# Performance work log

Hardware: AMD Instinct MI355X
Metric: run time of the kernel (lower is better)

The kernel has to match this reference:

```python
import jax, jax.numpy as jnp
import numpy as np
import math

MAX_DISP = 4
STRIDE = 1
PAD = MAX_DISP


def setup_inputs() -> dict:
    key = jax.random.key(0)
    k1, k2 = jax.random.split(key)
    B, C, H, W = 8, 128, 128, 192
    x1 = jax.random.normal(k1, (B, C, H, W), dtype=jnp.float32)
    x2 = jax.random.normal(k2, (B, C, H, W), dtype=jnp.float32)
    return {"x1": x1, "x2": x2}


def reference(x1, x2):
    B, C, H, W = x1.shape
    inv_sqrt_c = np.float32(1.0 / math.sqrt(C))
    # zero-pad x2 spatially by max_displacement on each side
    x2p = jnp.pad(x2, ((0, 0), (0, 0), (PAD, PAD), (PAD, PAD)))
    corrs = []
    # fixed small loop over the 80 displacements (structural, unrolled under jit)
    for i in range(-MAX_DISP, MAX_DISP + 1, STRIDE):
        for j in range(-MAX_DISP, MAX_DISP + 1, STRIDE):
            if i == 0 and j == 0:
                continue
            x2_slice = x2p[:, :, PAD + i:PAD + i + H, PAD + j:PAD + j + W]
            # per-pixel dot product over channels, scaled by 1/sqrt(C)
            corrs.append(jnp.sum(x1 * x2_slice, axis=1) * inv_sqrt_c)
    # [B, 80, H, W]
    return jnp.stack(corrs, axis=1)
```

## Files before the change

### kernel.cpp

```cpp
#include <hip/hip_runtime.h>


#define B_  8
#define C_  128
#define H_  128
#define W_  192
#define HW_ (H_*W_)
#define HALO 4
#define WT  32
#define HT  8
#define CC  8
#define X2R (HT + 2*HALO)
#define X2C (WT + 2*HALO)
#define X2SZ (X2R*X2C)
#define NTHREADS 576

__global__ __launch_bounds__(NTHREADS, 2) void corr_kernel(
    const float* __restrict__ x1, const float* __restrict__ x2,
    float* __restrict__ out)
{
    __shared__ float x2s[CC][X2SZ];

    const int tx = threadIdx.x;
    const int ty = threadIdx.y;
    const int iz = threadIdx.z;
    const int tid = tx + 8*ty + 64*iz;

    const int w0t = blockIdx.x * WT;
    const int h0t = blockIdx.y * HT;
    const int b   = blockIdx.z;

    const float* x1b = x1 + (size_t)b * C_ * HW_;
    const float* x2b = x2 + (size_t)b * C_ * HW_;

    const int e0 = tid;
    const int r0s = e0 / X2C, c0s = e0 - r0s * X2C;
    const int gh0 = h0t - HALO + r0s, gw0 = w0t - HALO + c0s;
    const bool inb0 = ((unsigned)gh0 < (unsigned)H_) & ((unsigned)gw0 < (unsigned)W_);
    const int g0 = gh0 * W_ + gw0;

    const int e1 = tid + NTHREADS;
    const bool has1 = (e1 < X2SZ);
    const int r1s = e1 / X2C, c1s = e1 - r1s * X2C;
    const int gh1 = h0t - HALO + r1s, gw1 = w0t - HALO + c1s;
    const bool inb1 = has1 & ((unsigned)gh1 < (unsigned)H_) & ((unsigned)gw1 < (unsigned)W_);
    const int g1 = gh1 * W_ + gw1;

    const float* x1t = x1b + (h0t + ty) * W_ + w0t + 4 * tx;
    const int woff = (ty + iz) * X2C + 4 * tx;

    float acc[9][4];
    #pragma unroll
    for (int j = 0; j < 9; j++)
        #pragma unroll
        for (int p = 0; p < 4; p++) acc[j][p] = 0.f;

    for (int c0 = 0; c0 < C_; c0 += CC) {
        __syncthreads();

        #pragma unroll
        for (int cc = 0; cc < CC; cc++) {
            const float* p = x2b + (size_t)(c0 + cc) * HW_;
            x2s[cc][e0] = inb0 ? p[g0] : 0.f;
            if (has1) x2s[cc][e1] = inb1 ? p[g1] : 0.f;
        }
        __syncthreads();

        #pragma unroll 2
        for (int cc = 0; cc < CC; cc++) {
            const float4 a = *(const float4*)(x1t + (size_t)(c0 + cc) * HW_);
            const float av[4] = {a.x, a.y, a.z, a.w};
            const float* row = &x2s[cc][woff];
            const float4 w0 = *(const float4*)(row);
            const float4 w1 = *(const float4*)(row + 4);
            const float4 w2 = *(const float4*)(row + 8);
            const float rr[12] = {w0.x, w0.y, w0.z, w0.w,
                                  w1.x, w1.y, w1.z, w1.w,
                                  w2.x, w2.y, w2.z, w2.w};
            #pragma unroll
            for (int j = 0; j < 9; j++)
                #pragma unroll
                for (int p = 0; p < 4; p++)
                    acc[j][p] = fmaf(av[p], rr[j + p], acc[j][p]);
        }
    }

    const float scale = 0.08838834764831845f;
    const int h  = h0t + ty;
    const int w0 = w0t + tx*4;
    float* outb = out + (size_t)b * 80 * HW_ + (size_t)h * W_ + w0;
    #pragma unroll
    for (int j = 0; j < 9; j++) {
        const int gi = iz * 9 + j;
        if (gi == 40) continue;
        const int ch = gi - (gi > 40 ? 1 : 0);
        float4 v;
        v.x = acc[j][0] * scale;
        v.y = acc[j][1] * scale;
        v.z = acc[j][2] * scale;
        v.w = acc[j][3] * scale;
        *(float4*)(outb + (size_t)ch * HW_) = v;
    }
}

extern "C" void kernel_launch(void* const* d_in, const int* in_sizes, int n_in,
                              void* d_out, int out_size, void* d_ws, size_t ws_size,
                              hipStream_t stream) {
    const float* x1 = (const float*)d_in[0];
    const float* x2 = (const float*)d_in[1];
    float* out = (float*)d_out;

    dim3 block(8, 8, 9);
    dim3 grid(W_ / WT, H_ / HT, B_);
    corr_kernel<<<grid, block, 0, stream>>>(x1, x2, out);
}
```

Before: 450.5 us.

## Double-buffer x2 halo tiles with float4 register prefetch and batch-interleaved grid

Replaces the synchronous per-chunk scalar load of the x2 halo tile with a two-buffer LDS scheme. The next chunk is fetched with float4 loads into registers while the current chunk is computed, then stored to the alternate buffer, so each chunk needs one barrier instead of two. The chunk is shrunk to 4 channels, and out-of-bounds halo slots are zeroed once up front. The grid is flattened with batch as the fastest index and launch bounds are raised for occupancy, at the cost of register pressure and possible spills.

```diff
diff --git a/kernel.cpp b/kernel.cpp
--- a/kernel.cpp
+++ b/kernel.cpp
@@ -9,42 +9,74 @@
 #define HALO 4
 #define WT  32
 #define HT  8
-#define CC  8
-#define X2R (HT + 2*HALO)
-#define X2C (WT + 2*HALO)
-#define X2SZ (X2R*X2C)
+#define CC  4
+#define NCHUNK (C_/CC)
+#define X2C 40
+#define X2SZ 640
+#define BUFSZ (CC*X2SZ)
 #define NTHREADS 576
 
-__global__ __launch_bounds__(NTHREADS, 2) void corr_kernel(
+__global__ __launch_bounds__(NTHREADS, 5) void corr_kernel(
     const float* __restrict__ x1, const float* __restrict__ x2,
     float* __restrict__ out)
 {
-    __shared__ float x2s[CC][X2SZ];
+    __shared__ float x2s[2][BUFSZ];
 
     const int tx = threadIdx.x;
     const int ty = threadIdx.y;
     const int iz = threadIdx.z;
     const int tid = tx + 8*ty + 64*iz;
 
-    const int w0t = blockIdx.x * WT;
-    const int h0t = blockIdx.y * HT;
-    const int b   = blockIdx.z;
+    const int bid   = blockIdx.x;
+    const int b     = bid & 7;
+    const int t     = bid >> 3;
+    const int w0t = (t % 6) * WT;
+    const int h0t = (t / 6) * HT;
 
     const float* x1b = x1 + (size_t)b * C_ * HW_;
     const float* x2b = x2 + (size_t)b * C_ * HW_;
 
-    const int e0 = tid;
-    const int r0s = e0 / X2C, c0s = e0 - r0s * X2C;
-    const int gh0 = h0t - HALO + r0s, gw0 = w0t - HALO + c0s;
-    const bool inb0 = ((unsigned)gh0 < (unsigned)H_) & ((unsigned)gw0 < (unsigned)W_);
-    const int g0 = gh0 * W_ + gw0;
+    const int e0  = tid;
+    const int ch0 = e0 / 160;
+    const int r0  = (e0 - 160*ch0) / 10;
+    const int cq0 = e0 - 160*ch0 - 10*r0;
+    const int gh0 = h0t - HALO + r0;
+    const int gw0 = w0t - HALO + 4*cq0;
+    const bool inb0 = ((unsigned)gh0 < (unsigned)H_) && ((unsigned)gw0 < (unsigned)W_);
+    const int  l0   = 4 * e0;
+    const float* ps0 = x2b + (inb0 ? ((long)ch0 * HW_ + (long)gh0 * W_ + gw0) : 0);
+    const long  st0 = inb0 ? (long)CC * HW_ : 0;
 
-    const int e1 = tid + NTHREADS;
-    const bool has1 = (e1 < X2SZ);
-    const int r1s = e1 / X2C, c1s = e1 - r1s * X2C;
-    const int gh1 = h0t - HALO + r1s, gw1 = w0t - HALO + c1s;
-    const bool inb1 = has1 & ((unsigned)gh1 < (unsigned)H_) & ((unsigned)gw1 < (unsigned)W_);
-    const int g1 = gh1 * W_ + gw1;
+    const int e1  = tid + NTHREADS;
+    const int ch1 = e1 / 160;
+    const int r1  = (e1 - 160*ch1) / 10;
+    const int cq1 = e1 - 160*ch1 - 10*r1;
+    const int gh1 = h0t - HALO + r1;
+    const int gw1 = w0t - HALO + 4*cq1;
+    const bool inb1 = ((unsigned)gh1 < (unsigned)H_) && ((unsigned)gw1 < (unsigned)W_);
+    const int  l1   = 4 * e1;
+    const float* ps1 = x2b + (inb1 ? ((long)ch1 * HW_ + (long)gh1 * W_ + gw1) : 0);
+    const long  st1 = inb1 ? (long)CC * HW_ : 0;
+
+    const float4 fz = make_float4(0.f, 0.f, 0.f, 0.f);
+    if (!inb0) {
+        *(float4*)&x2s[0][l0] = fz;
+        *(float4*)&x2s[1][l0] = fz;
+    }
+    if (iz == 0 && !inb1) {
+        *(float4*)&x2s[0][l1] = fz;
+        *(float4*)&x2s[1][l1] = fz;
+    }
+
+    {
+        const float4 t0 = *(const float4*)ps0;
+        if (inb0) *(float4*)&x2s[0][l0] = t0;
+        if (iz == 0) {
+            const float4 t1 = *(const float4*)ps1;
+            if (inb1) *(float4*)&x2s[0][l1] = t1;
+        }
+    }
+    __syncthreads();
 
     const float* x1t = x1b + (h0t + ty) * W_ + w0t + 4 * tx;
     const int woff = (ty + iz) * X2C + 4 * tx;
@@ -55,25 +87,30 @@
         #pragma unroll
         for (int p = 0; p < 4; p++) acc[j][p] = 0.f;
 
-    for (int c0 = 0; c0 < C_; c0 += CC) {
-        __syncthreads();
+    #pragma unroll 2
+    for (int k = 0; k < NCHUNK; ++k) {
+        const int cb = k * CC;
+        const bool more = (k + 1 < NCHUNK);
 
+        float4 a[CC];
         #pragma unroll
-        for (int cc = 0; cc < CC; cc++) {
-            const float* p = x2b + (size_t)(c0 + cc) * HW_;
-            x2s[cc][e0] = inb0 ? p[g0] : 0.f;
-            if (has1) x2s[cc][e1] = inb1 ? p[g1] : 0.f;
+        for (int cc = 0; cc < CC; ++cc)
+            a[cc] = *(const float4*)(x1t + (size_t)(cb + cc) * HW_);
+
+        float4 t0, t1;
+        if (more) {
+            t0 = *(const float4*)(ps0 + (long)(k + 1) * st0);
+            if (iz == 0) t1 = *(const float4*)(ps1 + (long)(k + 1) * st1);
         }
-        __syncthreads();
 
-        #pragma unroll 2
-        for (int cc = 0; cc < CC; cc++) {
-            const float4 a = *(const float4*)(x1t + (size_t)(c0 + cc) * HW_);
-            const float av[4] = {a.x, a.y, a.z, a.w};
-            const float* row = &x2s[cc][woff];
+        const float* buf = &x2s[k & 1][0];
+        #pragma unroll
+        for (int cc = 0; cc < CC; ++cc) {
+            const float* row = buf + cc * X2SZ + woff;
             const float4 w0 = *(const float4*)(row);
             const float4 w1 = *(const float4*)(row + 4);
             const float4 w2 = *(const float4*)(row + 8);
+            const float av[4] = {a[cc].x, a[cc].y, a[cc].z, a[cc].w};
             const float rr[12] = {w0.x, w0.y, w0.z, w0.w,
                                   w1.x, w1.y, w1.z, w1.w,
                                   w2.x, w2.y, w2.z, w2.w};
@@ -83,6 +120,14 @@
                 for (int p = 0; p < 4; p++)
                     acc[j][p] = fmaf(av[p], rr[j + p], acc[j][p]);
         }
+
+        if (more) {
+            float* dst = &x2s[(k & 1) ^ 1][0];
+            if (inb0) *(float4*)(dst + l0) = t0;
+            if (iz == 0 && inb1) *(float4*)(dst + l1) = t1;
+        }
+
+        __syncthreads();
     }
 
     const float scale = 0.08838834764831845f;
@@ -111,6 +156,6 @@
     float* out = (float*)d_out;
 
     dim3 block(8, 8, 9);
-    dim3 grid(W_ / WT, H_ / HT, B_);
+    dim3 grid(768, 1, 1);
     corr_kernel<<<grid, block, 0, stream>>>(x1, x2, out);
 }
```

After: 1.176 ms. 2.61x slower.

## Drop shared-memory staging and read x2 directly from global memory

Applied to the files above, without the earlier changes.

Removes the LDS tile of x2 and its two barriers per channel chunk, so each thread loads three float4 windows of x2 straight from global memory (zero-page pointer with zero stride for out-of-bounds). The grid is also flattened with batch as the fastest index so that neighbouring blocks share spatial tiles across batches. This relies on L1/L2 caching to absorb the 9x redundant x2 reads across iz threads instead of explicit LDS reuse, which adds global load traffic in exchange for removing the sync overhead.

```diff
diff --git a/kernel.cpp b/kernel.cpp
--- a/kernel.cpp
+++ b/kernel.cpp
@@ -6,48 +6,48 @@
 #define H_  128
 #define W_  192
 #define HW_ (H_*W_)
-#define HALO 4
 #define WT  32
 #define HT  8
-#define CC  8
-#define X2R (HT + 2*HALO)
-#define X2C (WT + 2*HALO)
-#define X2SZ (X2R*X2C)
 #define NTHREADS 576
+
+__device__ static const __attribute__((aligned(16))) float g_zero[4] = {0.f, 0.f, 0.f, 0.f};
 
 __global__ __launch_bounds__(NTHREADS, 2) void corr_kernel(
     const float* __restrict__ x1, const float* __restrict__ x2,
     float* __restrict__ out)
 {
-    __shared__ float x2s[CC][X2SZ];
-
     const int tx = threadIdx.x;
     const int ty = threadIdx.y;
     const int iz = threadIdx.z;
-    const int tid = tx + 8*ty + 64*iz;
 
-    const int w0t = blockIdx.x * WT;
-    const int h0t = blockIdx.y * HT;
-    const int b   = blockIdx.z;
+    const int bid = blockIdx.x;
+    const int b   = bid & 7;
+    const int t   = bid >> 3;
+    const int w0t = (t % 6) * WT;
+    const int h0t = (t / 6) * HT;
 
     const float* x1b = x1 + (size_t)b * C_ * HW_;
     const float* x2b = x2 + (size_t)b * C_ * HW_;
 
-    const int e0 = tid;
-    const int r0s = e0 / X2C, c0s = e0 - r0s * X2C;
-    const int gh0 = h0t - HALO + r0s, gw0 = w0t - HALO + c0s;
-    const bool inb0 = ((unsigned)gh0 < (unsigned)H_) & ((unsigned)gw0 < (unsigned)W_);
-    const int g0 = gh0 * W_ + gw0;
+    const int h_out = h0t + ty;
+    const int w_out = w0t + 4 * tx;
 
-    const int e1 = tid + NTHREADS;
-    const bool has1 = (e1 < X2SZ);
-    const int r1s = e1 / X2C, c1s = e1 - r1s * X2C;
-    const int gh1 = h0t - HALO + r1s, gw1 = w0t - HALO + c1s;
-    const bool inb1 = has1 & ((unsigned)gh1 < (unsigned)H_) & ((unsigned)gw1 < (unsigned)W_);
-    const int g1 = gh1 * W_ + gw1;
+    const float* x1p = x1b + (size_t)h_out * W_ + w_out;
 
-    const float* x1t = x1b + (h0t + ty) * W_ + w0t + 4 * tx;
-    const int woff = (ty + iz) * X2C + 4 * tx;
+    const int r2 = h_out + iz - 4;
+    const bool rowok = ((unsigned)r2 < (unsigned)H_);
+    const int c0 = w_out - 4, c1 = w_out, c2 = w_out + 4;
+    const bool ok0 = rowok && ((unsigned)c0 < (unsigned)W_);
+    const bool ok1 = rowok;
+    const bool ok2 = rowok && ((unsigned)c2 < (unsigned)W_);
+
+    const float* zp = g_zero;
+    const float* p0 = ok0 ? (x2b + (size_t)r2 * W_ + c0) : zp;
+    const float* p1 = ok1 ? (x2b + (size_t)r2 * W_ + c1) : zp;
+    const float* p2 = ok2 ? (x2b + (size_t)r2 * W_ + c2) : zp;
+    const int s0 = ok0 ? HW_ : 0;
+    const int s1 = ok1 ? HW_ : 0;
+    const int s2 = ok2 ? HW_ : 0;
 
     float acc[9][4];
     #pragma unroll
@@ -55,40 +55,27 @@
         #pragma unroll
         for (int p = 0; p < 4; p++) acc[j][p] = 0.f;
 
-    for (int c0 = 0; c0 < C_; c0 += CC) {
-        __syncthreads();
+    #pragma unroll 2
+    for (int c = 0; c < C_; ++c) {
+        const float4 a  = *(const float4*)(x1p);
+        const float4 w0 = *(const float4*)(p0);
+        const float4 w1 = *(const float4*)(p1);
+        const float4 w2 = *(const float4*)(p2);
+        x1p += HW_; p0 += s0; p1 += s1; p2 += s2;
 
+        const float av[4] = {a.x, a.y, a.z, a.w};
+        const float rr[12] = {w0.x, w0.y, w0.z, w0.w,
+                              w1.x, w1.y, w1.z, w1.w,
+                              w2.x, w2.y, w2.z, w2.w};
         #pragma unroll
-        for (int cc = 0; cc < CC; cc++) {
-            const float* p = x2b + (size_t)(c0 + cc) * HW_;
-            x2s[cc][e0] = inb0 ? p[g0] : 0.f;
-            if (has1) x2s[cc][e1] = inb1 ? p[g1] : 0.f;
-        }
-        __syncthreads();
-
-        #pragma unroll 2
-        for (int cc = 0; cc < CC; cc++) {
-            const float4 a = *(const float4*)(x1t + (size_t)(c0 + cc) * HW_);
-            const float av[4] = {a.x, a.y, a.z, a.w};
-            const float* row = &x2s[cc][woff];
-            const float4 w0 = *(const float4*)(row);
-            const float4 w1 = *(const float4*)(row + 4);
-            const float4 w2 = *(const float4*)(row + 8);
-            const float rr[12] = {w0.x, w0.y, w0.z, w0.w,
-                                  w1.x, w1.y, w1.z, w1.w,
-                                  w2.x, w2.y, w2.z, w2.w};
+        for (int j = 0; j < 9; j++)
             #pragma unroll
-            for (int j = 0; j < 9; j++)
-                #pragma unroll
-                for (int p = 0; p < 4; p++)
-                    acc[j][p] = fmaf(av[p], rr[j + p], acc[j][p]);
-        }
+            for (int p = 0; p < 4; p++)
+                acc[j][p] = fmaf(av[p], rr[j + p], acc[j][p]);
     }
 
     const float scale = 0.08838834764831845f;
-    const int h  = h0t + ty;
-    const int w0 = w0t + tx*4;
-    float* outb = out + (size_t)b * 80 * HW_ + (size_t)h * W_ + w0;
+    float* outb = out + (size_t)b * 80 * HW_ + (size_t)h_out * W_ + w_out;
     #pragma unroll
     for (int j = 0; j < 9; j++) {
         const int gi = iz * 9 + j;
@@ -111,6 +98,6 @@
     float* out = (float*)d_out;
 
     dim3 block(8, 8, 9);
-    dim3 grid(W_ / WT, H_ / HT, B_);
+    dim3 grid(768, 1, 1);
     corr_kernel<<<grid, block, 0, stream>>>(x1, x2, out);
 }
```

Measured after the change: 496.4 us. 1.1x slower.
